# Kernel optimization log

Measured on AMD Instinct MI355X. Metric: run time of the kernel, lower is better.

## Reference

```python
import jax, jax.numpy as jnp
import numpy as np

B, S, M, H, NH, FF = 8, 512, 512, 1024, 16, 4096
DH = H // NH      # 64
K = M + S         # key length = mem_len + sentence_len
EPS = 1e-5


def setup_inputs() -> dict:
    key = jax.random.key(0)
    ks = jax.random.split(key, 14)
    p = lambda k, shp: jax.random.normal(k, shp, jnp.float32) * 0.02
    return {
        "token_embedding": jax.random.normal(ks[0], (B, S, H), jnp.float32),
        "rel_pos_embedding": jax.random.normal(ks[1], (K, H), jnp.float32),
        "mems": jax.random.normal(ks[2], (B, M, H), jnp.float32),
        "segment_num": 1,
        "layer_num": 0,
        "Wq": p(ks[3], (H, H)), "Wk": p(ks[4], (H, H)), "Wv": p(ks[5], (H, H)),
        "Wr": p(ks[6], (H, H)), "Wo": p(ks[7], (H, H)),
        "u_bias": p(ks[8], (NH, DH)), "v_bias": p(ks[9], (NH, DH)),
        "gamma": jnp.ones((H,), jnp.float32), "beta": jnp.zeros((H,), jnp.float32),
        "W1": p(ks[10], (H, FF)), "b1": jnp.zeros((FF,), jnp.float32),
        "W2": p(ks[11], (FF, H)), "b2": jnp.zeros((H,), jnp.float32),
    }


def _rel_shift(x):
    # Transformer-XL relative shift. x: [B, NH, S, K]
    b, nh, s, k = x.shape
    x = jnp.pad(x, ((0, 0), (0, 0), (0, 0), (1, 0)))          # [B,NH,S,K+1]
    x = x.reshape(b, nh, k + 1, s)[:, :, 1:, :]               # drop first row
    return x.reshape(b, nh, s, k)


def _layer_norm(x, gamma, beta):
    mu = jnp.mean(x, axis=-1, keepdims=True)
    var = jnp.mean(jnp.square(x - mu), axis=-1, keepdims=True)
    return (x - mu) / jnp.sqrt(var + EPS) * gamma + beta


def reference(token_embedding, rel_pos_embedding, mems, segment_num, layer_num,
              Wq, Wk, Wv, Wr, Wo, u_bias, v_bias, gamma, beta, W1, b1, W2, b2):
    x = token_embedding                                   # [B,S,H]
    cat = jnp.concatenate([mems, x], axis=1)              # [B,K,H]
    q = (x @ Wq).reshape(B, S, NH, DH)
    k = (cat @ Wk).reshape(B, K, NH, DH)
    v = (cat @ Wv).reshape(B, K, NH, DH)
    r = (rel_pos_embedding @ Wr).reshape(K, NH, DH)
    # content + position terms (Transformer-XL)
    AC = jnp.einsum('bsnd,bknd->bnsk', q + u_bias, k)
    BD = _rel_shift(jnp.einsum('bsnd,knd->bnsk', q + v_bias, r))
    scores = (AC + BD) / jnp.sqrt(jnp.float32(DH))        # [B,NH,S,K]
    # causal mask with memory: query i sees keys j <= i + mem_len
    i = jnp.arange(S)[:, None]
    j = jnp.arange(K)[None, :]
    scores = jnp.where(j <= i + M, scores, jnp.float32(-1e9))
    attn = jax.nn.softmax(scores, axis=-1)
    ctx = jnp.einsum('bnsk,bknd->bsnd', attn, v).reshape(B, S, H)
    attn_out = ctx @ Wo
    # residual + LN
    h = _layer_norm(attn_out + x, gamma, beta)
    # FFN (relu), residual + LN (same LN params reused, as in source)
    ff = jax.nn.relu(h @ W1 + b1) @ W2 + b2
    y = _layer_norm(ff + h, gamma, beta)
    new_mems = jax.lax.stop_gradient(cat[:, -M:])
    return y, new_mems
```

## Files before the change

kernel.cpp:

```cpp
#include <hip/hip_runtime.h>


typedef float  floatx4 __attribute__((ext_vector_type(4)));
typedef __bf16 bf16x8  __attribute__((ext_vector_type(8)));
typedef __bf16 bf16x4  __attribute__((ext_vector_type(4)));

#define MFMA16(a, b, c) __builtin_amdgcn_mfma_f32_16x16x32_bf16((a), (b), (c), 0, 0, 0)
#define CFENCE() __asm__ __volatile__("" ::: "memory")

typedef __attribute__((address_space(1))) void gv_t;
typedef __attribute__((address_space(3))) void lv_t;

__device__ __forceinline__ void g2l16(const void* g, void* l) {
  __builtin_amdgcn_global_load_lds((gv_t*)g, (lv_t*)l, 16, 0, 0);
}

__device__ __forceinline__ floatx4 zf4() { floatx4 z = {0.f, 0.f, 0.f, 0.f}; return z; }

template <int CTRL>
__device__ __forceinline__ float dppf(float v) {
  return __builtin_bit_cast(
      float, __builtin_amdgcn_mov_dpp(__builtin_bit_cast(int, v), CTRL, 0xF, 0xF, true));
}
__device__ __forceinline__ float red16_max(float x) {
  x = fmaxf(x, dppf<0xB1>(x));
  x = fmaxf(x, dppf<0x4E>(x));
  x = fmaxf(x, dppf<0x124>(x));
  x = fmaxf(x, dppf<0x128>(x));
  return x;
}
__device__ __forceinline__ float red16_sum(float x) {
  x += dppf<0xB1>(x);
  x += dppf<0x4E>(x);
  x += dppf<0x124>(x);
  x += dppf<0x128>(x);
  return x;
}

__device__ __forceinline__ bool in_is_bf16(const void* gamma_raw) {
  return *(const unsigned*)gamma_raw == 0x3F803F80u;
}

struct F8 { float v[8]; };

__device__ __forceinline__ F8 load8(const void* p, size_t i, bool bf) {
  F8 r;
  if (bf) {
    bf16x8 t = *(const bf16x8*)((const __bf16*)p + i);
#pragma unroll
    for (int j = 0; j < 8; j++) r.v[j] = (float)t[j];
  } else {
    floatx4 a = *(const floatx4*)((const float*)p + i);
    floatx4 b = *(const floatx4*)((const float*)p + i + 4);
#pragma unroll
    for (int j = 0; j < 4; j++) { r.v[j] = a[j]; r.v[4 + j] = b[j]; }
  }
  return r;
}

__device__ __forceinline__ void store8b(__bf16* p, size_t i, F8 r) {
  bf16x8 t;
#pragma unroll
  for (int j = 0; j < 8; j++) t[j] = (__bf16)r.v[j];
  *(bf16x8*)(p + i) = t;
}

__device__ __forceinline__ void store8raw(void* p, size_t i, F8 r, bool bf) {
  if (bf) {
    store8b((__bf16*)p, i, r);
  } else {
    floatx4 a, b;
#pragma unroll
    for (int j = 0; j < 4; j++) { a[j] = r.v[j]; b[j] = r.v[4 + j]; }
    *(floatx4*)((float*)p + i) = a;
    *(floatx4*)((float*)p + i + 4) = b;
  }
}

enum { EP_PLAIN = 0, EP_ADDRES = 2, EP_BIAS_RELU = 3, EP_BIAS_RES = 4 };

template <int MODE, int BM>
__global__ __launch_bounds__(256) void gemm_bt(
    const __bf16* __restrict__ A, const __bf16* __restrict__ Bt,
    __bf16* __restrict__ C, const float* __restrict__ bias1,
    const __bf16* __restrict__ res, int M, int N, int K) {
  constexpr int FR = BM / 32;
  constexpr int PA = BM / 32;
  __shared__ __attribute__((aligned(16))) __bf16 As[BM * 64];
  __shared__ __attribute__((aligned(16))) __bf16 Bs[128 * 64];
  const int t = threadIdx.x;
  const int lane = t & 63, w = t >> 6;
  const int l15 = lane & 15, quad = lane >> 4;
  const int row0 = blockIdx.y * BM, col0 = blockIdx.x * 128;

  floatx4 acc[FR][4];
#pragma unroll
  for (int i = 0; i < FR; i++)
#pragma unroll
    for (int j = 0; j < 4; j++) acc[i][j] = zf4();

  const __bf16* gAsrc[PA];
  const __bf16* gBsrc[4];
#pragma unroll
  for (int p = 0; p < PA; p++) {
    const int i = t + p * 256, row = i >> 3, c8 = i & 7;
    gAsrc[p] = A + (size_t)(row0 + row) * K + ((c8 ^ (row & 7)) << 3);
  }
#pragma unroll
  for (int p = 0; p < 4; p++) {
    const int i = t + p * 256, row = i >> 3, c8 = i & 7;
    gBsrc[p] = Bt + (size_t)(col0 + row) * K + ((c8 ^ (row & 7)) << 3);
  }

  const int wr = (w >> 1) * (BM / 2), wc = (w & 1) * 64;
  const int swz = l15 & 7;

  for (int kk = 0; kk < K; kk += 64) {
#pragma unroll
    for (int p = 0; p < PA; p++) g2l16(gAsrc[p] + kk, As + (size_t)(t + p * 256) * 8);
#pragma unroll
    for (int p = 0; p < 4; p++) g2l16(gBsrc[p] + kk, Bs + (size_t)(t + p * 256) * 8);
    __syncthreads();
#pragma unroll
    for (int ks = 0; ks < 2; ks++) {
      const int ch = ((ks << 2) | quad) ^ swz;
      bf16x8 af[FR], bfr[4];
#pragma unroll
      for (int fr = 0; fr < FR; fr++)
        af[fr] = *(const bf16x8*)(As + (wr + fr * 16 + l15) * 64 + ch * 8);
#pragma unroll
      for (int fc = 0; fc < 4; fc++)
        bfr[fc] = *(const bf16x8*)(Bs + (wc + fc * 16 + l15) * 64 + ch * 8);
#pragma unroll
      for (int fr = 0; fr < FR; fr++)
#pragma unroll
        for (int fc = 0; fc < 4; fc++) acc[fr][fc] = MFMA16(af[fr], bfr[fc], acc[fr][fc]);
    }
    __syncthreads();
  }

#pragma unroll
  for (int fr = 0; fr < FR; fr++) {
#pragma unroll
    for (int fc = 0; fc < 4; fc++) {
#pragma unroll
      for (int r = 0; r < 4; r++) {
        const int row = row0 + wr + fr * 16 + quad * 4 + r;
        const int col = col0 + wc + fc * 16 + l15;
        const size_t idx = (size_t)row * N + col;
        const float v = acc[fr][fc][r];
        if (MODE == EP_ADDRES) {
          C[idx] = (__bf16)(v + (float)res[idx]);
        } else if (MODE == EP_BIAS_RELU) {
          float u = v + bias1[col];
          C[idx] = (__bf16)(u > 0.f ? u : 0.f);
        } else if (MODE == EP_BIAS_RES) {
          C[idx] = (__bf16)(v + bias1[col] + (float)res[idx]);
        } else {
          C[idx] = (__bf16)v;
        }
      }
    }
  }
}

__global__ __launch_bounds__(256) void proj_gemm(
    const __bf16* __restrict__ xb, const __bf16* __restrict__ catb,
    const __bf16* __restrict__ relb, const __bf16* __restrict__ WqT,
    const __bf16* __restrict__ WkT, const __bf16* __restrict__ WvT,
    const __bf16* __restrict__ WrT, __bf16* __restrict__ qb,
    __bf16* __restrict__ kb, __bf16* __restrict__ vtb, __bf16* __restrict__ rbo) {
  const int tid = (int)(blockIdx.x & 7) * 168 + (int)(blockIdx.x >> 3);
  const __bf16 *A, *Bt;
  __bf16* C;
  int local;
  bool isV = false;
  if (tid < 256)       { A = xb;   Bt = WqT; C = qb;  local = tid; }
  else if (tid < 768)  { A = catb; Bt = WkT; C = kb;  local = tid - 256; }
  else if (tid < 1280) { A = catb; Bt = WvT; C = vtb; local = tid - 768; isV = true; }
  else                 { A = relb; Bt = WrT; C = rbo; local = tid - 1280; }
  const int row0 = (local >> 3) * 128, col0 = (local & 7) * 128;

  __shared__ __attribute__((aligned(16))) __bf16 As[128 * 64];
  __shared__ __attribute__((aligned(16))) __bf16 Bs[128 * 64];
  const int t = threadIdx.x;
  const int lane = t & 63, w = t >> 6;
  const int l15 = lane & 15, quad = lane >> 4;

  floatx4 acc[4][4];
#pragma unroll
  for (int i = 0; i < 4; i++)
#pragma unroll
    for (int j = 0; j < 4; j++) acc[i][j] = zf4();

  const __bf16* gAsrc[4];
  const __bf16* gBsrc[4];
#pragma unroll
  for (int p = 0; p < 4; p++) {
    const int i = t + p * 256, row = i >> 3, c8 = i & 7;
    gAsrc[p] = A + (((size_t)(row0 + row)) << 10) + ((c8 ^ (row & 7)) << 3);
    gBsrc[p] = Bt + (((size_t)(col0 + row)) << 10) + ((c8 ^ (row & 7)) << 3);
  }

  const int wr = (w >> 1) * 64, wc = (w & 1) * 64;
  const int swz = l15 & 7;

  for (int kk = 0; kk < 1024; kk += 64) {
#pragma unroll
    for (int p = 0; p < 4; p++) g2l16(gAsrc[p] + kk, As + (size_t)(t + p * 256) * 8);
#pragma unroll
    for (int p = 0; p < 4; p++) g2l16(gBsrc[p] + kk, Bs + (size_t)(t + p * 256) * 8);
    __syncthreads();
#pragma unroll
    for (int ks = 0; ks < 2; ks++) {
      const int ch = ((ks << 2) | quad) ^ swz;
      bf16x8 af[4], bfr[4];
#pragma unroll
      for (int fr = 0; fr < 4; fr++)
        af[fr] = *(const bf16x8*)(As + (wr + fr * 16 + l15) * 64 + ch * 8);
#pragma unroll
      for (int fc = 0; fc < 4; fc++)
        bfr[fc] = *(const bf16x8*)(Bs + (wc + fc * 16 + l15) * 64 + ch * 8);
#pragma unroll
      for (int fr = 0; fr < 4; fr++)
#pragma unroll
        for (int fc = 0; fc < 4; fc++) acc[fr][fc] = MFMA16(af[fr], bfr[fc], acc[fr][fc]);
    }
    __syncthreads();
  }

  if (isV) {
#pragma unroll
    for (int fr = 0; fr < 4; fr++) {
      const int row = row0 + wr + fr * 16 + quad * 4;
      const int b_ = row >> 10;
      const int pos = row & 1023;
#pragma unroll
      for (int fc = 0; fc < 4; fc++) {
        const int col = col0 + wc + fc * 16 + l15;
        bf16x4 pk;
#pragma unroll
        for (int r = 0; r < 4; r++) pk[r] = (__bf16)acc[fr][fc][r];
        *(bf16x4*)(C + (((size_t)(b_ * 1024 + col)) << 10) + pos) = pk;
      }
    }
  } else {
#pragma unroll
    for (int fr = 0; fr < 4; fr++) {
#pragma unroll
      for (int fc = 0; fc < 4; fc++) {
#pragma unroll
        for (int r = 0; r < 4; r++) {
          const int row = row0 + wr + fr * 16 + quad * 4 + r;
          const int col = col0 + wc + fc * 16 + l15;
          C[((size_t)row << 10) + col] = (__bf16)acc[fr][fc][r];
        }
      }
    }
  }
}

__global__ __launch_bounds__(256, 4) void attn_kernel(
    const __bf16* __restrict__ qb, const __bf16* __restrict__ kb,
    const __bf16* __restrict__ vtb, const __bf16* __restrict__ rb,
    const float* __restrict__ uf, const float* __restrict__ vf,
    __bf16* __restrict__ ctx) {
  __shared__ __attribute__((aligned(16))) __bf16 qL[64 * 72];
  __shared__ __attribute__((aligned(16))) __bf16 kL[64 * 72];
  __shared__ __attribute__((aligned(16))) __bf16 vtL[64 * 72];
  __shared__ __attribute__((aligned(16))) __bf16 pS[4 * 1152];

  const int t = threadIdx.x;
  const int lane = t & 63, w = t >> 6;
  const int l15 = lane & 15, quad = lane >> 4;
  const int i0 = (int)((blockIdx.x + blockIdx.z) & 7) * 64;
  const int n = blockIdx.y;
  const int b = blockIdx.z;

  {
    const int r = t >> 2, c = (t & 3) * 8;
    const size_t g = ((size_t)(b * 512 + i0 + r) << 10) + (n << 6) + c;
    *(bf16x8*)(qL + r * 72 + c) = *(const bf16x8*)(qb + g);
    *(bf16x8*)(qL + r * 72 + c + 32) = *(const bf16x8*)(qb + g + 32);
  }

  floatx4 o[4];
  float mrun[4], lrun[4];
#pragma unroll
  for (int i = 0; i < 4; i++) { o[i] = zf4(); mrun[i] = -1e30f; lrun[i] = 0.f; }

  bf16x8 aqu[2], aqv[2];
  __bf16* pp = pS + w * 1152;

  const int jmax = i0 + 512;
  for (int j0 = 0; j0 <= jmax; j0 += 64) {
    {
      const int r = t >> 2, c = (t & 3) * 8;
      const size_t gk = ((size_t)(b * 1024 + j0 + r) << 10) + (n << 6) + c;
      *(bf16x8*)(kL + r * 72 + c) = *(const bf16x8*)(kb + gk);
      *(bf16x8*)(kL + r * 72 + c + 32) = *(const bf16x8*)(kb + gk + 32);
      const size_t gv = ((size_t)((b * 16 + n) * 64 + r) << 10) + j0 + c;
      bf16x8 v8a = *(const bf16x8*)(vtb + gv);
      bf16x8 v8b = *(const bf16x8*)(vtb + gv + 32);
      const int sw = ((r >> 3) & 3) << 1;
      *(bf16x8*)(vtL + r * 72 + (((c >> 3) ^ sw) << 3)) = v8a;
      *(bf16x8*)(vtL + r * 72 + ((((c >> 3) + 4) ^ sw) << 3)) = v8b;
    }
    __syncthreads();

    if (j0 == 0) {
#pragma unroll
      for (int ks = 0; ks < 2; ks++) {
        bf16x8 qf = *(const bf16x8*)(qL + (16 * w + l15) * 72 + ks * 32 + quad * 8);
        const int dbase = (n << 6) + ks * 32 + quad * 8;
#pragma unroll
        for (int j = 0; j < 8; j++) {
          const float qv_ = (float)qf[j];
          aqu[ks][j] = (__bf16)(qv_ + uf[dbase + j]);
          aqv[ks][j] = (__bf16)(qv_ + vf[dbase + j]);
        }
      }
    }

    floatx4 s[4];
#pragma unroll
    for (int cf = 0; cf < 4; cf++) s[cf] = zf4();
#pragma unroll
    for (int ks = 0; ks < 2; ks++)
#pragma unroll
      for (int cf = 0; cf < 4; cf++) {
        bf16x8 bfr = *(const bf16x8*)(kL + (cf * 16 + l15) * 72 + ks * 32 + quad * 8);
        s[cf] = MFMA16(aqu[ks], bfr, s[cf]);
      }

    floatx4 bnd[5];
#pragma unroll
    for (int i = 0; i < 5; i++) bnd[i] = zf4();
    const int bw = j0 - i0 - 16 * w + 496;
#pragma unroll
    for (int ks = 0; ks < 2; ks++)
#pragma unroll
      for (int cf2 = 0; cf2 < 5; cf2++) {
        int rel = bw + cf2 * 16 + l15;
        rel = rel > 1023 ? 1023 : rel;
        bf16x8 bfr = *(const bf16x8*)(rb + ((size_t)rel << 10) + (n << 6) + ks * 32 + quad * 8);
        bnd[cf2] = MFMA16(aqv[ks], bfr, bnd[cf2]);
      }

    const bool mt = (j0 == jmax);
#pragma unroll
    for (int r = 0; r < 4; r++) {
      const int li = quad * 4 + r;
      const int tt = l15 + 15 - li;
      const int src = (quad << 4) | (tt & 15);
      float pm[5];
#pragma unroll
      for (int c5 = 0; c5 < 5; c5++) pm[c5] = __shfl(bnd[c5][r], src);
      const bool hi = (tt >> 4) != 0;
#pragma unroll
      for (int cf = 0; cf < 4; cf++) {
        const float bd = hi ? pm[cf + 1] : pm[cf];
        float sv = (s[cf][r] + bd) * 0.125f;
        if (mt && (cf * 16 + l15) > 16 * w + li) sv = -1e9f;
        s[cf][r] = sv;
      }
    }

    float alpha[4], mnew[4];
#pragma unroll
    for (int r = 0; r < 4; r++) {
      float mx = fmaxf(fmaxf(s[0][r], s[1][r]), fmaxf(s[2][r], s[3][r]));
      mx = red16_max(mx);
      mnew[r] = fmaxf(mrun[r], mx);
      alpha[r] = __expf(mrun[r] - mnew[r]);
      mrun[r] = mnew[r];
    }
#pragma unroll
    for (int cf = 0; cf < 4; cf++)
#pragma unroll
      for (int r = 0; r < 4; r++) s[cf][r] = __expf(s[cf][r] - mnew[r]);
#pragma unroll
    for (int r = 0; r < 4; r++) {
      float rs = s[0][r] + s[1][r] + s[2][r] + s[3][r];
      rs = red16_sum(rs);
      lrun[r] = lrun[r] * alpha[r] + rs;
    }
#pragma unroll
    for (int of = 0; of < 4; of++) {
      floatx4 ov = o[of];
#pragma unroll
      for (int r = 0; r < 4; r++) ov[r] *= alpha[r];
      o[of] = ov;
    }

#pragma unroll
    for (int cf = 0; cf < 4; cf++)
#pragma unroll
      for (int r = 0; r < 4; r++)
        pp[(quad * 4 + r) * 72 + cf * 16 + l15] = (__bf16)s[cf][r];
    CFENCE();
#pragma unroll
    for (int ks = 0; ks < 2; ks++) {
      bf16x8 pa = *(const bf16x8*)(pp + l15 * 72 + ks * 32 + quad * 8);
#pragma unroll
      for (int of = 0; of < 4; of++) {
        const int row = of * 16 + l15;
        const int kbx = (ks * 4 + quad) ^ (((row >> 3) & 3) << 1);
        bf16x8 bv = *(const bf16x8*)(vtL + row * 72 + kbx * 8);
        o[of] = MFMA16(pa, bv, o[of]);
      }
    }
    __syncthreads();
  }

#pragma unroll
  for (int r = 0; r < 4; r++) {
    const float inv = 1.f / lrun[r];
    const int row = i0 + 16 * w + quad * 4 + r;
#pragma unroll
    for (int of = 0; of < 4; of++)
      ctx[((size_t)(b * 512 + row) << 10) + (n << 6) + of * 16 + l15] =
          (__bf16)(o[of][r] * inv);
  }
}

template <int RAW>
__global__ __launch_bounds__(256) void ln_kernel(
    const __bf16* __restrict__ in, const float* __restrict__ gf,
    const float* __restrict__ bf_, __bf16* __restrict__ outb,
    void* __restrict__ outraw, const void* __restrict__ gamma_raw) {
  const int t = threadIdx.x;
  const int lane = t & 63, w = t >> 6;
  const size_t row = (size_t)blockIdx.x * 4 + w;
  const __bf16* p = in + (row << 10) + lane * 16;
  bf16x8 v0 = *(const bf16x8*)(p);
  bf16x8 v1 = *(const bf16x8*)(p + 8);
  float f[16];
#pragma unroll
  for (int j = 0; j < 8; j++) { f[j] = (float)v0[j]; f[8 + j] = (float)v1[j]; }
  float s = 0.f, ss = 0.f;
#pragma unroll
  for (int j = 0; j < 16; j++) { s += f[j]; ss += f[j] * f[j]; }
#pragma unroll
  for (int d = 1; d < 64; d <<= 1) { s += __shfl_xor(s, d); ss += __shfl_xor(ss, d); }
  const float mu = s * (1.f / 1024.f);
  const float var = ss * (1.f / 1024.f) - mu * mu;
  const float rstd = rsqrtf(var + 1e-5f);
  float gv[16], bv[16];
#pragma unroll
  for (int j = 0; j < 16; j += 4) {
    floatx4 g = *(const floatx4*)(gf + lane * 16 + j);
    floatx4 bb = *(const floatx4*)(bf_ + lane * 16 + j);
#pragma unroll
    for (int q = 0; q < 4; q++) { gv[j + q] = g[q]; bv[j + q] = bb[q]; }
  }
  float r[16];
#pragma unroll
  for (int j = 0; j < 16; j++) r[j] = (f[j] - mu) * rstd * gv[j] + bv[j];

  if (RAW == 0) {
    bf16x8 o0, o1;
#pragma unroll
    for (int j = 0; j < 8; j++) { o0[j] = (__bf16)r[j]; o1[j] = (__bf16)r[8 + j]; }
    *(bf16x8*)(outb + (row << 10) + lane * 16) = o0;
    *(bf16x8*)(outb + (row << 10) + lane * 16 + 8) = o1;
  } else {
    const bool bf = in_is_bf16(gamma_raw);
    if (bf) {
      __bf16* o = (__bf16*)outraw;
      bf16x8 o0, o1;
#pragma unroll
      for (int j = 0; j < 8; j++) { o0[j] = (__bf16)r[j]; o1[j] = (__bf16)r[8 + j]; }
      *(bf16x8*)(o + (row << 10) + lane * 16) = o0;
      *(bf16x8*)(o + (row << 10) + lane * 16 + 8) = o1;
    } else {
      float* o = (float*)outraw + (row << 10) + lane * 16;
#pragma unroll
      for (int j = 0; j < 16; j += 4) {
        floatx4 q;
#pragma unroll
        for (int k = 0; k < 4; k++) q[k] = r[j + k];
        *(floatx4*)(o + j) = q;
      }
    }
  }
}

__global__ __launch_bounds__(256) void prep_kernel(
    const void* __restrict__ x, const void* __restrict__ mems,
    const void* __restrict__ relp, const void* __restrict__ gamma_raw,
    __bf16* __restrict__ catb, __bf16* __restrict__ xb,
    __bf16* __restrict__ relb, void* __restrict__ dout) {
  const bool bf = in_is_bf16(gamma_raw);
  const size_t idx = (size_t)blockIdx.x * 256 + threadIdx.x;
  if (idx < 1048576) {
    const size_t e = idx * 8;
    const int rowk = (int)(e >> 10);
    const int col = (int)(e & 1023);
    const int b = rowk >> 10, pos = rowk & 1023;
    F8 v = (pos < 512)
               ? load8(mems, (((size_t)(b * 512 + pos)) << 10) + col, bf)
               : load8(x, (((size_t)(b * 512 + pos - 512)) << 10) + col, bf);
    store8b(catb, e, v);
  } else if (idx < 1572864) {
    const size_t e = (idx - 1048576) * 8;
    store8b(xb, e, load8(x, e, bf));
  } else if (idx < 1703936) {
    const size_t e = (idx - 1572864) * 8;
    store8b(relb, e, load8(relp, e, bf));
  } else {
    const size_t e = (idx - 1703936) * 8;
    store8raw(dout, (size_t)4194304 + e, load8(x, e, bf), bf);
  }
}

__global__ __launch_bounds__(256) void bias_conv_kernel(
    const void* ub, const void* vb, const void* b1, const void* b2,
    const void* gamma, const void* beta, const void* gamma_raw,
    float* __restrict__ dst) {
  const bool bf = in_is_bf16(gamma_raw);
  const int j = blockIdx.x * 256 + threadIdx.x;
  const void* src;
  int k;
  if (j < 1024)        { src = ub;    k = j; }
  else if (j < 2048)   { src = vb;    k = j - 1024; }
  else if (j < 6144)   { src = b1;    k = j - 2048; }
  else if (j < 7168)   { src = b2;    k = j - 6144; }
  else if (j < 8192)   { src = gamma; k = j - 7168; }
  else if (j < 9216)   { src = beta;  k = j - 8192; }
  else return;
  dst[j] = bf ? (float)((const __bf16*)src)[k] : ((const float*)src)[k];
}

__device__ __forceinline__ void transpose_tile(
    const void* __restrict__ W, __bf16* __restrict__ Wt, int K, int N,
    int k0, int n0, bool bf, __bf16* tile) {
  const int t = threadIdx.x;
  const int r = t >> 2, c = (t & 3) * 8;
  F8 a = load8(W, (size_t)(k0 + r) * N + n0 + c, bf);
  F8 b = load8(W, (size_t)(k0 + r) * N + n0 + c + 32, bf);
  bf16x8 ta, tb;
#pragma unroll
  for (int j = 0; j < 8; j++) { ta[j] = (__bf16)a.v[j]; tb[j] = (__bf16)b.v[j]; }
  *(bf16x8*)(tile + r * 72 + c) = ta;
  *(bf16x8*)(tile + r * 72 + c + 32) = tb;
  __syncthreads();
  bf16x8 o0, o1;
#pragma unroll
  for (int j = 0; j < 8; j++) {
    o0[j] = tile[(c + j) * 72 + r];
    o1[j] = tile[(c + 32 + j) * 72 + r];
  }
  *(bf16x8*)(Wt + (size_t)(n0 + r) * K + k0 + c) = o0;
  *(bf16x8*)(Wt + (size_t)(n0 + r) * K + k0 + c + 32) = o1;
}

__global__ __launch_bounds__(256) void qkvro_transpose_kernel(
    const void* __restrict__ Wq, const void* __restrict__ Wk,
    const void* __restrict__ Wv, const void* __restrict__ Wr,
    const void* __restrict__ Wo, const void* __restrict__ gamma_raw,
    __bf16* __restrict__ WqT, __bf16* __restrict__ WkT,
    __bf16* __restrict__ WvT, __bf16* __restrict__ WrT,
    __bf16* __restrict__ WoT) {
  __shared__ __attribute__((aligned(16))) __bf16 tile[64 * 72];
  const bool bf = in_is_bf16(gamma_raw);
  const void* W;
  __bf16* Wt;
  switch (blockIdx.z) {
    case 0: W = Wq; Wt = WqT; break;
    case 1: W = Wk; Wt = WkT; break;
    case 2: W = Wv; Wt = WvT; break;
    case 3: W = Wr; Wt = WrT; break;
    default: W = Wo; Wt = WoT; break;
  }
  transpose_tile(W, Wt, 1024, 1024, blockIdx.y * 64, blockIdx.x * 64, bf, tile);
}

__global__ __launch_bounds__(256) void big_transpose_kernel(
    const void* __restrict__ W1, const void* __restrict__ W2,
    const void* __restrict__ gamma_raw, __bf16* __restrict__ W1T,
    __bf16* __restrict__ W2T) {
  __shared__ __attribute__((aligned(16))) __bf16 tile[64 * 72];
  const bool bf = in_is_bf16(gamma_raw);
  const int bx = blockIdx.x, by = blockIdx.y;
  if (blockIdx.z == 0) {
    transpose_tile(W1, W1T, 1024, 4096, by * 64, bx * 64, bf, tile);
  } else {
    transpose_tile(W2, W2T, 4096, 1024, (by * 4 + (bx >> 4)) * 64, (bx & 15) * 64,
                   bf, tile);
  }
}

extern "C" void kernel_launch(void* const* d_in, const int* in_sizes, int n_in,
                              void* d_out, int out_size, void* d_ws, size_t ws_size,
                              hipStream_t stream) {
  const void* x = d_in[0];
  const void* relp = d_in[1];
  const void* mems = d_in[2];
  const void* Wq = d_in[5];
  const void* Wk = d_in[6];
  const void* Wv = d_in[7];
  const void* Wr = d_in[8];
  const void* Wo = d_in[9];
  const void* ub = d_in[10];
  const void* vbias = d_in[11];
  const void* gamma = d_in[12];
  const void* beta = d_in[13];
  const void* W1 = d_in[14];
  const void* b1 = d_in[15];
  const void* W2 = d_in[16];
  const void* b2 = d_in[17];

  char* ws = (char*)d_ws;
  const size_t MB = (size_t)1 << 20;
  __bf16* catb = (__bf16*)(ws);
  __bf16* ctx  = (__bf16*)(ws);
  __bf16* ff1  = (__bf16*)(ws);
  __bf16* kb   = (__bf16*)(ws + 16 * MB);
  __bf16* vtb  = (__bf16*)(ws + 32 * MB);
  __bf16* ao   = (__bf16*)(ws + 32 * MB);
  __bf16* hb   = (__bf16*)(ws + 40 * MB);
  __bf16* qb   = (__bf16*)(ws + 48 * MB);
  __bf16* ff2  = (__bf16*)(ws + 48 * MB);
  __bf16* xb   = (__bf16*)(ws + 56 * MB);
  __bf16* W1T  = (__bf16*)(ws + 56 * MB);
  __bf16* relb = (__bf16*)(ws + 64 * MB);
  __bf16* rb   = (__bf16*)(ws + 66 * MB);
  __bf16* WqT  = (__bf16*)(ws + 68 * MB);
  __bf16* WkT  = (__bf16*)(ws + 70 * MB);
  __bf16* W2T  = (__bf16*)(ws + 64 * MB);
  __bf16* WvT  = (__bf16*)(ws + 72 * MB);
  __bf16* WrT  = (__bf16*)(ws + 74 * MB);
  __bf16* WoT  = (__bf16*)(ws + 76 * MB);
  float*  uf   = (float*)(ws + 78 * MB);
  float*  vf   = uf + 1024;
  float*  b1f  = uf + 2048;
  float*  b2f  = uf + 6144;
  float*  gf   = uf + 7168;
  float*  betf = uf + 8192;

  prep_kernel<<<dim3(8704), 256, 0, stream>>>(x, mems, relp, gamma, catb, xb, relb, d_out);
  bias_conv_kernel<<<dim3(36), 256, 0, stream>>>(ub, vbias, b1, b2, gamma, beta, gamma, uf);
  qkvro_transpose_kernel<<<dim3(16, 16, 5), 256, 0, stream>>>(
      Wq, Wk, Wv, Wr, Wo, gamma, WqT, WkT, WvT, WrT, WoT);

  proj_gemm<<<dim3(1344), 256, 0, stream>>>(xb, catb, relb, WqT, WkT, WvT, WrT,
                                            qb, kb, vtb, rb);

  attn_kernel<<<dim3(8, 16, 8), 256, 0, stream>>>(qb, kb, vtb, rb, uf, vf, ctx);

  gemm_bt<EP_ADDRES, 64><<<dim3(8, 64), 256, 0, stream>>>(ctx, WoT, ao, nullptr, xb,
                                                          4096, 1024, 1024);
  ln_kernel<0><<<dim3(1024), 256, 0, stream>>>(ao, gf, betf, hb, nullptr, nullptr);

  big_transpose_kernel<<<dim3(64, 16, 2), 256, 0, stream>>>(W1, W2, gamma, W1T, W2T);

  gemm_bt<EP_BIAS_RELU, 128><<<dim3(32, 32), 256, 0, stream>>>(hb, W1T, ff1, b1f,
                                                               nullptr, 4096, 4096, 1024);
  gemm_bt<EP_BIAS_RES, 64><<<dim3(8, 64), 256, 0, stream>>>(ff1, W2T, ff2, b2f, hb,
                                                            4096, 1024, 4096);
  ln_kernel<1><<<dim3(1024), 256, 0, stream>>>(ff2, gf, betf, nullptr, d_out, gamma);

  (void)in_sizes; (void)n_in; (void)out_size; (void)ws_size;
}
```

Baseline: 496.6 us.

## Merge prep kernels, fuse LN1 with weight transpose, add BK template to GEMM

Three preprocessing launches (input conversion, bias conversion, QKVRO weight transpose) become one ingest kernel indexed by block ID. The first LayerNorm and the W1/W2 transpose now share a single launch. The GEMM gains a BK template parameter so the N=1024 GEMMs use a 128-wide K tile, halving their K-loop iterations and barriers at the cost of more LDS per block. The attention kernel's launch-bounds occupancy hint drops from 4 to 3 blocks, which allows more registers per thread.

```diff
diff --git a/kernel.cpp b/kernel.cpp
--- a/kernel.cpp
+++ b/kernel.cpp
@@ -79,15 +79,18 @@
 
 enum { EP_PLAIN = 0, EP_ADDRES = 2, EP_BIAS_RELU = 3, EP_BIAS_RES = 4 };
 
-template <int MODE, int BM>
+template <int MODE, int BM, int BK>
 __global__ __launch_bounds__(256) void gemm_bt(
     const __bf16* __restrict__ A, const __bf16* __restrict__ Bt,
     __bf16* __restrict__ C, const float* __restrict__ bias1,
     const __bf16* __restrict__ res, int M, int N, int K) {
   constexpr int FR = BM / 32;
-  constexpr int PA = BM / 32;
-  __shared__ __attribute__((aligned(16))) __bf16 As[BM * 64];
-  __shared__ __attribute__((aligned(16))) __bf16 Bs[128 * 64];
+  constexpr int NC = BK / 8;
+  constexpr int PA = (BM * NC) / 256;
+  constexpr int PB = (128 * NC) / 256;
+  constexpr int KS = BK / 32;
+  __shared__ __attribute__((aligned(16))) __bf16 As[BM * BK];
+  __shared__ __attribute__((aligned(16))) __bf16 Bs[128 * BK];
   const int t = threadIdx.x;
   const int lane = t & 63, w = t >> 6;
   const int l15 = lane & 15, quad = lane >> 4;
@@ -100,37 +103,37 @@
     for (int j = 0; j < 4; j++) acc[i][j] = zf4();
 
   const __bf16* gAsrc[PA];
-  const __bf16* gBsrc[4];
+  const __bf16* gBsrc[PB];
 #pragma unroll
   for (int p = 0; p < PA; p++) {
-    const int i = t + p * 256, row = i >> 3, c8 = i & 7;
-    gAsrc[p] = A + (size_t)(row0 + row) * K + ((c8 ^ (row & 7)) << 3);
-  }
-#pragma unroll
-  for (int p = 0; p < 4; p++) {
-    const int i = t + p * 256, row = i >> 3, c8 = i & 7;
-    gBsrc[p] = Bt + (size_t)(col0 + row) * K + ((c8 ^ (row & 7)) << 3);
+    const int i = t + p * 256, row = i / NC, c8 = i % NC;
+    gAsrc[p] = A + (size_t)(row0 + row) * K + ((c8 ^ (row & (NC - 1))) << 3);
+  }
+#pragma unroll
+  for (int p = 0; p < PB; p++) {
+    const int i = t + p * 256, row = i / NC, c8 = i % NC;
+    gBsrc[p] = Bt + (size_t)(col0 + row) * K + ((c8 ^ (row & (NC - 1))) << 3);
   }
 
   const int wr = (w >> 1) * (BM / 2), wc = (w & 1) * 64;
-  const int swz = l15 & 7;
-
-  for (int kk = 0; kk < K; kk += 64) {
+  const int swz = l15 & (NC - 1);
+
+  for (int kk = 0; kk < K; kk += BK) {
 #pragma unroll
     for (int p = 0; p < PA; p++) g2l16(gAsrc[p] + kk, As + (size_t)(t + p * 256) * 8);
 #pragma unroll
-    for (int p = 0; p < 4; p++) g2l16(gBsrc[p] + kk, Bs + (size_t)(t + p * 256) * 8);
+    for (int p = 0; p < PB; p++) g2l16(gBsrc[p] + kk, Bs + (size_t)(t + p * 256) * 8);
     __syncthreads();
 #pragma unroll
-    for (int ks = 0; ks < 2; ks++) {
+    for (int ks = 0; ks < KS; ks++) {
       const int ch = ((ks << 2) | quad) ^ swz;
       bf16x8 af[FR], bfr[4];
 #pragma unroll
       for (int fr = 0; fr < FR; fr++)
-        af[fr] = *(const bf16x8*)(As + (wr + fr * 16 + l15) * 64 + ch * 8);
+        af[fr] = *(const bf16x8*)(As + (size_t)(wr + fr * 16 + l15) * BK + ch * 8);
 #pragma unroll
       for (int fc = 0; fc < 4; fc++)
-        bfr[fc] = *(const bf16x8*)(Bs + (wc + fc * 16 + l15) * 64 + ch * 8);
+        bfr[fc] = *(const bf16x8*)(Bs + (size_t)(wc + fc * 16 + l15) * BK + ch * 8);
 #pragma unroll
       for (int fr = 0; fr < FR; fr++)
 #pragma unroll
@@ -260,7 +263,7 @@
   }
 }
 
-__global__ __launch_bounds__(256, 4) void attn_kernel(
+__global__ __launch_bounds__(256, 3) void attn_kernel(
     const __bf16* __restrict__ qb, const __bf16* __restrict__ kb,
     const __bf16* __restrict__ vtb, const __bf16* __restrict__ rb,
     const float* __restrict__ uf, const float* __restrict__ vf,
@@ -424,14 +427,9 @@
   }
 }
 
-template <int RAW>
-__global__ __launch_bounds__(256) void ln_kernel(
-    const __bf16* __restrict__ in, const float* __restrict__ gf,
-    const float* __restrict__ bf_, __bf16* __restrict__ outb,
-    void* __restrict__ outraw, const void* __restrict__ gamma_raw) {
-  const int t = threadIdx.x;
-  const int lane = t & 63, w = t >> 6;
-  const size_t row = (size_t)blockIdx.x * 4 + w;
+__device__ __forceinline__ void ln_row(const __bf16* in, const float* gf,
+                                       const float* bf_, size_t row, int lane,
+                                       float* r) {
   const __bf16* p = in + (row << 10) + lane * 16;
   bf16x8 v0 = *(const bf16x8*)(p);
   bf16x8 v1 = *(const bf16x8*)(p + 8);
@@ -446,90 +444,42 @@
   const float mu = s * (1.f / 1024.f);
   const float var = ss * (1.f / 1024.f) - mu * mu;
   const float rstd = rsqrtf(var + 1e-5f);
-  float gv[16], bv[16];
 #pragma unroll
   for (int j = 0; j < 16; j += 4) {
     floatx4 g = *(const floatx4*)(gf + lane * 16 + j);
     floatx4 bb = *(const floatx4*)(bf_ + lane * 16 + j);
 #pragma unroll
-    for (int q = 0; q < 4; q++) { gv[j + q] = g[q]; bv[j + q] = bb[q]; }
-  }
+    for (int q = 0; q < 4; q++) r[j + q] = (f[j + q] - mu) * rstd * g[q] + bb[q];
+  }
+}
+
+__global__ __launch_bounds__(256) void ln_raw_kernel(
+    const __bf16* __restrict__ in, const float* __restrict__ gf,
+    const float* __restrict__ bf_, void* __restrict__ outraw,
+    const void* __restrict__ gamma_raw) {
+  const int t = threadIdx.x;
+  const int lane = t & 63, w = t >> 6;
+  const size_t row = (size_t)blockIdx.x * 4 + w;
   float r[16];
-#pragma unroll
-  for (int j = 0; j < 16; j++) r[j] = (f[j] - mu) * rstd * gv[j] + bv[j];
-
-  if (RAW == 0) {
+  ln_row(in, gf, bf_, row, lane, r);
+  const bool bf = in_is_bf16(gamma_raw);
+  if (bf) {
+    __bf16* o = (__bf16*)outraw;
     bf16x8 o0, o1;
 #pragma unroll
     for (int j = 0; j < 8; j++) { o0[j] = (__bf16)r[j]; o1[j] = (__bf16)r[8 + j]; }
-    *(bf16x8*)(outb + (row << 10) + lane * 16) = o0;
-    *(bf16x8*)(outb + (row << 10) + lane * 16 + 8) = o1;
+    *(bf16x8*)(o + (row << 10) + lane * 16) = o0;
+    *(bf16x8*)(o + (row << 10) + lane * 16 + 8) = o1;
   } else {
-    const bool bf = in_is_bf16(gamma_raw);
-    if (bf) {
-      __bf16* o = (__bf16*)outraw;
-      bf16x8 o0, o1;
-#pragma unroll
-      for (int j = 0; j < 8; j++) { o0[j] = (__bf16)r[j]; o1[j] = (__bf16)r[8 + j]; }
-      *(bf16x8*)(o + (row << 10) + lane * 16) = o0;
-      *(bf16x8*)(o + (row << 10) + lane * 16 + 8) = o1;
-    } else {
-      float* o = (float*)outraw + (row << 10) + lane * 16;
-#pragma unroll
-      for (int j = 0; j < 16; j += 4) {
-        floatx4 q;
-#pragma unroll
-        for (int k = 0; k < 4; k++) q[k] = r[j + k];
-        *(floatx4*)(o + j) = q;
-      }
-    }
-  }
-}
-
-__global__ __launch_bounds__(256) void prep_kernel(
-    const void* __restrict__ x, const void* __restrict__ mems,
-    const void* __restrict__ relp, const void* __restrict__ gamma_raw,
-    __bf16* __restrict__ catb, __bf16* __restrict__ xb,
-    __bf16* __restrict__ relb, void* __restrict__ dout) {
-  const bool bf = in_is_bf16(gamma_raw);
-  const size_t idx = (size_t)blockIdx.x * 256 + threadIdx.x;
-  if (idx < 1048576) {
-    const size_t e = idx * 8;
-    const int rowk = (int)(e >> 10);
-    const int col = (int)(e & 1023);
-    const int b = rowk >> 10, pos = rowk & 1023;
-    F8 v = (pos < 512)
-               ? load8(mems, (((size_t)(b * 512 + pos)) << 10) + col, bf)
-               : load8(x, (((size_t)(b * 512 + pos - 512)) << 10) + col, bf);
-    store8b(catb, e, v);
-  } else if (idx < 1572864) {
-    const size_t e = (idx - 1048576) * 8;
-    store8b(xb, e, load8(x, e, bf));
-  } else if (idx < 1703936) {
-    const size_t e = (idx - 1572864) * 8;
-    store8b(relb, e, load8(relp, e, bf));
-  } else {
-    const size_t e = (idx - 1703936) * 8;
-    store8raw(dout, (size_t)4194304 + e, load8(x, e, bf), bf);
-  }
-}
-
-__global__ __launch_bounds__(256) void bias_conv_kernel(
-    const void* ub, const void* vb, const void* b1, const void* b2,
-    const void* gamma, const void* beta, const void* gamma_raw,
-    float* __restrict__ dst) {
-  const bool bf = in_is_bf16(gamma_raw);
-  const int j = blockIdx.x * 256 + threadIdx.x;
-  const void* src;
-  int k;
-  if (j < 1024)        { src = ub;    k = j; }
-  else if (j < 2048)   { src = vb;    k = j - 1024; }
-  else if (j < 6144)   { src = b1;    k = j - 2048; }
-  else if (j < 7168)   { src = b2;    k = j - 6144; }
-  else if (j < 8192)   { src = gamma; k = j - 7168; }
-  else if (j < 9216)   { src = beta;  k = j - 8192; }
-  else return;
-  dst[j] = bf ? (float)((const __bf16*)src)[k] : ((const float*)src)[k];
+    float* o = (float*)outraw + (row << 10) + lane * 16;
+#pragma unroll
+    for (int j = 0; j < 16; j += 4) {
+      floatx4 q;
+#pragma unroll
+      for (int k = 0; k < 4; k++) q[k] = r[j + k];
+      *(floatx4*)(o + j) = q;
+    }
+  }
 }
 
 __device__ __forceinline__ void transpose_tile(
@@ -555,39 +505,103 @@
   *(bf16x8*)(Wt + (size_t)(n0 + r) * K + k0 + c + 32) = o1;
 }
 
-__global__ __launch_bounds__(256) void qkvro_transpose_kernel(
-    const void* __restrict__ Wq, const void* __restrict__ Wk,
-    const void* __restrict__ Wv, const void* __restrict__ Wr,
-    const void* __restrict__ Wo, const void* __restrict__ gamma_raw,
+__global__ __launch_bounds__(256) void ingest_kernel(
+    const void* __restrict__ x, const void* __restrict__ mems,
+    const void* __restrict__ relp, const void* __restrict__ Wq,
+    const void* __restrict__ Wk, const void* __restrict__ Wv,
+    const void* __restrict__ Wr, const void* __restrict__ Wo,
+    const void* __restrict__ ub, const void* __restrict__ vbias,
+    const void* __restrict__ b1, const void* __restrict__ b2,
+    const void* __restrict__ gamma, const void* __restrict__ beta,
+    __bf16* __restrict__ catb, __bf16* __restrict__ xb,
+    __bf16* __restrict__ relb, void* __restrict__ dout,
     __bf16* __restrict__ WqT, __bf16* __restrict__ WkT,
     __bf16* __restrict__ WvT, __bf16* __restrict__ WrT,
-    __bf16* __restrict__ WoT) {
+    __bf16* __restrict__ WoT, float* __restrict__ uf) {
   __shared__ __attribute__((aligned(16))) __bf16 tile[64 * 72];
-  const bool bf = in_is_bf16(gamma_raw);
-  const void* W;
-  __bf16* Wt;
-  switch (blockIdx.z) {
-    case 0: W = Wq; Wt = WqT; break;
-    case 1: W = Wk; Wt = WkT; break;
-    case 2: W = Wv; Wt = WvT; break;
-    case 3: W = Wr; Wt = WrT; break;
-    default: W = Wo; Wt = WoT; break;
-  }
-  transpose_tile(W, Wt, 1024, 1024, blockIdx.y * 64, blockIdx.x * 64, bf, tile);
-}
-
-__global__ __launch_bounds__(256) void big_transpose_kernel(
+  const bool bf = in_is_bf16(gamma);
+  const int bid = blockIdx.x;
+  const int t = threadIdx.x;
+  if (bid < 8704) {
+    const size_t idx = (size_t)bid * 256 + t;
+    if (idx < 1048576) {
+      const size_t e = idx * 8;
+      const int rowk = (int)(e >> 10);
+      const int col = (int)(e & 1023);
+      const int b = rowk >> 10, pos = rowk & 1023;
+      F8 v = (pos < 512)
+                 ? load8(mems, (((size_t)(b * 512 + pos)) << 10) + col, bf)
+                 : load8(x, (((size_t)(b * 512 + pos - 512)) << 10) + col, bf);
+      store8b(catb, e, v);
+    } else if (idx < 1572864) {
+      const size_t e = (idx - 1048576) * 8;
+      store8b(xb, e, load8(x, e, bf));
+    } else if (idx < 1703936) {
+      const size_t e = (idx - 1572864) * 8;
+      store8b(relb, e, load8(relp, e, bf));
+    } else {
+      const size_t e = (idx - 1703936) * 8;
+      store8raw(dout, (size_t)4194304 + e, load8(x, e, bf), bf);
+    }
+  } else if (bid < 9984) {
+    const int e = bid - 8704;
+    const int z = e >> 8;
+    const int ti = e & 255;
+    const void* W;
+    __bf16* Wt;
+    switch (z) {
+      case 0: W = Wq; Wt = WqT; break;
+      case 1: W = Wk; Wt = WkT; break;
+      case 2: W = Wv; Wt = WvT; break;
+      case 3: W = Wr; Wt = WrT; break;
+      default: W = Wo; Wt = WoT; break;
+    }
+    transpose_tile(W, Wt, 1024, 1024, (ti >> 4) * 64, (ti & 15) * 64, bf, tile);
+  } else {
+    const int j = (bid - 9984) * 256 + t;
+    const void* src;
+    int k;
+    if (j < 1024)        { src = ub;    k = j; }
+    else if (j < 2048)   { src = vbias; k = j - 1024; }
+    else if (j < 6144)   { src = b1;    k = j - 2048; }
+    else if (j < 7168)   { src = b2;    k = j - 6144; }
+    else if (j < 8192)   { src = gamma; k = j - 7168; }
+    else                 { src = beta;  k = j - 8192; }
+    uf[j] = bf ? (float)((const __bf16*)src)[k] : ((const float*)src)[k];
+  }
+}
+
+__global__ __launch_bounds__(256) void ln1_bigt_kernel(
+    const __bf16* __restrict__ ao, const float* __restrict__ gf,
+    const float* __restrict__ bf_, __bf16* __restrict__ hb,
     const void* __restrict__ W1, const void* __restrict__ W2,
     const void* __restrict__ gamma_raw, __bf16* __restrict__ W1T,
     __bf16* __restrict__ W2T) {
   __shared__ __attribute__((aligned(16))) __bf16 tile[64 * 72];
-  const bool bf = in_is_bf16(gamma_raw);
-  const int bx = blockIdx.x, by = blockIdx.y;
-  if (blockIdx.z == 0) {
-    transpose_tile(W1, W1T, 1024, 4096, by * 64, bx * 64, bf, tile);
+  const int bid = blockIdx.x;
+  const int t = threadIdx.x;
+  if (bid < 1024) {
+    const int lane = t & 63, w = t >> 6;
+    const size_t row = (size_t)bid * 4 + w;
+    float r[16];
+    ln_row(ao, gf, bf_, row, lane, r);
+    bf16x8 o0, o1;
+#pragma unroll
+    for (int j = 0; j < 8; j++) { o0[j] = (__bf16)r[j]; o1[j] = (__bf16)r[8 + j]; }
+    *(bf16x8*)(hb + (row << 10) + lane * 16) = o0;
+    *(bf16x8*)(hb + (row << 10) + lane * 16 + 8) = o1;
   } else {
-    transpose_tile(W2, W2T, 4096, 1024, (by * 4 + (bx >> 4)) * 64, (bx & 15) * 64,
-                   bf, tile);
+    const bool bf = in_is_bf16(gamma_raw);
+    const int e = bid - 1024;
+    const int z = e >> 10;
+    const int ti = e & 1023;
+    const int bx = ti & 63, by = ti >> 6;
+    if (z == 0) {
+      transpose_tile(W1, W1T, 1024, 4096, by * 64, bx * 64, bf, tile);
+    } else {
+      transpose_tile(W2, W2T, 4096, 1024, (by * 4 + (bx >> 4)) * 64, (bx & 15) * 64,
+                     bf, tile);
+    }
   }
 }
 
@@ -633,33 +647,32 @@
   __bf16* WrT  = (__bf16*)(ws + 74 * MB);
   __bf16* WoT  = (__bf16*)(ws + 76 * MB);
   float*  uf   = (float*)(ws + 78 * MB);
-  float*  vf   = uf + 1024;
   float*  b1f  = uf + 2048;
   float*  b2f  = uf + 6144;
   float*  gf   = uf + 7168;
   float*  betf = uf + 8192;
-
-  prep_kernel<<<dim3(8704), 256, 0, stream>>>(x, mems, relp, gamma, catb, xb, relb, d_out);
-  bias_conv_kernel<<<dim3(36), 256, 0, stream>>>(ub, vbias, b1, b2, gamma, beta, gamma, uf);
-  qkvro_transpose_kernel<<<dim3(16, 16, 5), 256, 0, stream>>>(
-      Wq, Wk, Wv, Wr, Wo, gamma, WqT, WkT, WvT, WrT, WoT);
+  float*  vf   = uf + 1024;
+
+  ingest_kernel<<<dim3(10020), 256, 0, stream>>>(
+      x, mems, relp, Wq, Wk, Wv, Wr, Wo, ub, vbias, b1, b2, gamma, beta,
+      catb, xb, relb, d_out, WqT, WkT, WvT, WrT, WoT, uf);
 
   proj_gemm<<<dim3(1344), 256, 0, stream>>>(xb, catb, relb, WqT, WkT, WvT, WrT,
                                             qb, kb, vtb, rb);
 
   attn_kernel<<<dim3(8, 16, 8), 256, 0, stream>>>(qb, kb, vtb, rb, uf, vf, ctx);
 
-  gemm_bt<EP_ADDRES, 64><<<dim3(8, 64), 256, 0, stream>>>(ctx, WoT, ao, nullptr, xb,
-                                                          4096, 1024, 1024);
-  ln_kernel<0><<<dim3(1024), 256, 0, stream>>>(ao, gf, betf, hb, nullptr, nullptr);
-
-  big_transpose_kernel<<<dim3(64, 16, 2), 256, 0, stream>>>(W1, W2, gamma, W1T, W2T);
-
-  gemm_bt<EP_BIAS_RELU, 128><<<dim3(32, 32), 256, 0, stream>>>(hb, W1T, ff1, b1f,
-                                                               nullptr, 4096, 4096, 1024);
-  gemm_bt<EP_BIAS_RES, 64><<<dim3(8, 64), 256, 0, stream>>>(ff1, W2T, ff2, b2f, hb,
-                                                            4096, 1024, 4096);
-  ln_kernel<1><<<dim3(1024), 256, 0, stream>>>(ff2, gf, betf, nullptr, d_out, gamma);
+  gemm_bt<EP_ADDRES, 64, 128><<<dim3(8, 64), 256, 0, stream>>>(
+      ctx, WoT, ao, nullptr, xb, 4096, 1024, 1024);
+
+  ln1_bigt_kernel<<<dim3(3072), 256, 0, stream>>>(ao, gf, betf, hb, W1, W2, gamma,
+                                                  W1T, W2T);
+
+  gemm_bt<EP_BIAS_RELU, 128, 64><<<dim3(32, 32), 256, 0, stream>>>(
+      hb, W1T, ff1, b1f, nullptr, 4096, 4096, 1024);
+  gemm_bt<EP_BIAS_RES, 64, 128><<<dim3(8, 64), 256, 0, stream>>>(
+      ff1, W2T, ff2, b2f, hb, 4096, 1024, 4096);
+  ln_raw_kernel<<<dim3(1024), 256, 0, stream>>>(ff2, gf, betf, d_out, gamma);
 
   (void)in_sizes; (void)n_in; (void)out_size; (void)ws_size;
 }
```

Measured after the change: 485.1 us. 1.02x faster.
